# Kernel optimization log

Measured on AMD Instinct MI355X. Metric: run time of the kernel, lower is better.

## Reference

```python
import jax, jax.numpy as jnp
import numpy as np

K_NEIGHBORS = 3  # init kwarg k_neighbors


def setup_inputs() -> dict:
    key = jax.random.key(0)
    k1, k2 = jax.random.split(key)
    q = jax.random.normal(k1, (75, 640, 21, 21), dtype=jnp.float32)
    S = jax.random.normal(k2, (5, 640, 21, 21), dtype=jnp.float32)
    return {"q": q, "S": S, "qAV_num": 1, "SAV_num": 1, "shot_num": 1}


def reference(q, S, qAV_num, SAV_num, shot_num):
    B, C = q.shape[0], q.shape[1]
    # [B, HW, C], L2-normalize each local descriptor over channels
    qd = q.reshape(B, C, -1).transpose(0, 2, 1)
    qd = qd / jnp.linalg.norm(qd, axis=2, keepdims=True)

    N = S.shape[0]
    sd = S.reshape(N, C, -1).transpose(0, 2, 1)  # [N, HW, C]
    sd = sd / jnp.linalg.norm(sd, axis=2, keepdims=True)
    HW = sd.shape[1]
    M = SAV_num * shot_num * HW
    # group support images into classes: [ncls, C, M]
    sup = sd.reshape(-1, M, C).transpose(0, 2, 1)
    ncls = sup.shape[0]

    # cosine similarity: [B, ncls, HW, M]
    ip = jnp.einsum('bqc,ncm->bnqm', qd, sup)
    # split AV groups: [B//qAV, qAV, ncls, HW, M]
    ip = ip.reshape(B // qAV_num, qAV_num, ncls, HW, M)
    # top-k along the query-descriptor (HW) axis (torch dim=-2)
    topk = jax.lax.top_k(jnp.swapaxes(ip, -1, -2), K_NEIGHBORS)[0]  # [..., M, k]
    img2class = topk.sum(axis=(-1, -2))  # [B', qAV, ncls]
    # geometric mean over the AV axis (dim=1)
    sim = jnp.exp(jnp.mean(jnp.log(img2class), axis=1))  # [B', ncls]
    return sim
```

## Files before the change

### kernel.cpp

```cpp
#include <hip/hip_runtime.h>
#include <hip/hip_bf16.h>


#define B_IMGS 75
#define N_CLS  5
#define C_DIM  640
#define HW     441
#define HWP    448
#define NKT    20
#define NRB    28
#define CHUNK  512

typedef __attribute__((ext_vector_type(8))) short  short8;
typedef __attribute__((ext_vector_type(4))) float  float4v;

__device__ __forceinline__ void ins3(float& t0, float& t1, float& t2, float v) {
    float m  = fminf(t0, v);
    t0 = fmaxf(t0, v);
    float m2 = fminf(t1, m);
    t1 = fmaxf(t1, m);
    t2 = fmaxf(t2, m2);
}

__global__ __launch_bounds__(256)
void prep_kernel(const float* __restrict__ q, const float* __restrict__ S,
                 __hip_bfloat16* __restrict__ qn2, __hip_bfloat16* __restrict__ sn2,
                 float* __restrict__ out) {
    __shared__ float part[4][64];
    __shared__ float inv[64];

    int bid = blockIdx.x;
    if (bid == 0) {
        for (int i = threadIdx.x; i < B_IMGS * N_CLS; i += 256) out[i] = 0.f;
    }

    int img = bid / 7;
    int h0  = bid % 7;
    const float* src; __hip_bfloat16* dst;
    if (img < B_IMGS) {
        src = q + (size_t)img * C_DIM * HW;
        dst = qn2 + (size_t)img * NRB * NKT * CHUNK;
    } else {
        src = S + (size_t)(img - B_IMGS) * C_DIM * HW;
        dst = sn2 + (size_t)(img - B_IMGS) * NRB * NKT * CHUNK;
    }
    int t  = threadIdx.x;
    int hl = t & 63;
    int p  = t >> 6;
    int hw = h0 * 64 + hl;
    int hwc = (hw < HW) ? hw : (HW - 1);

    float ss = 0.f;
    for (int c0 = p * 160; c0 < (p + 1) * 160; c0 += 16) {
        float v[16];
#pragma unroll
        for (int j = 0; j < 16; ++j) v[j] = src[(size_t)(c0 + j) * HW + hwc];
#pragma unroll
        for (int j = 0; j < 16; ++j) ss += v[j] * v[j];
    }
    part[p][hl] = ss;
    __syncthreads();
    if (t < 64) {
        float tot = part[0][t] + part[1][t] + part[2][t] + part[3][t];
        inv[t] = (h0 * 64 + t < HW) ? rsqrtf(tot) : 0.f;
    }
    __syncthreads();

    int tl  = hl;
    int row = tl & 15;
    int oct = tl >> 4;
    int rb  = h0 * 4 + p;
    int hw2 = h0 * 64 + p * 16 + row;
    int hw2c = (hw2 < HW) ? hw2 : (HW - 1);
    float iv = inv[p * 16 + row];
    const float* s2 = src + hw2c;
#pragma unroll 2
    for (int kt = 0; kt < NKT; ++kt) {
        float v[8];
#pragma unroll
        for (int j = 0; j < 8; ++j)
            v[j] = s2[(size_t)(kt * 32 + oct * 8 + j) * HW];
        short8 o;
#pragma unroll
        for (int j = 0; j < 8; ++j) {
            __hip_bfloat16 h = __float2bfloat16(v[j] * iv);
            o[j] = *(short*)&h;
        }
        *(short8*)(dst + ((size_t)rb * NKT + kt) * CHUNK + tl * 8) = o;
    }
}

#define LOADSET(aS, bS, kt)                                                     \
    {                                                                           \
        _Pragma("unroll")                                                       \
        for (int r = 0; r < 7; ++r)                                             \
            aS[r] = *(const short8*)(pA + ((size_t)(r * 4 + w) * NKT + (kt)) * CHUNK); \
        _Pragma("unroll")                                                       \
        for (int j = 0; j < 4; ++j)                                             \
            bS[j] = *(const short8*)(pB + ((size_t)j * NKT + (kt)) * CHUNK);    \
    }

#define MFMASET(aS, bS)                                                         \
    {                                                                           \
        _Pragma("unroll")                                                       \
        for (int r = 0; r < 7; ++r)                                             \
            _Pragma("unroll")                                                   \
            for (int j = 0; j < 4; ++j)                                         \
                acc[r][j] = __builtin_amdgcn_mfma_f32_16x16x32_bf16(            \
                    aS[r], bS[j], acc[r][j], 0, 0, 0);                          \
    }

__global__ __launch_bounds__(256, 2)
void gemm_top3_kernel(const __hip_bfloat16* __restrict__ qn2,
                      const __hip_bfloat16* __restrict__ sn2,
                      float* __restrict__ out) {
    __shared__ float mrg[4][64][3];

    int id  = blockIdx.x;
    int xcd = id & 7;
    int j8  = id >> 3;
    int b   = (j8 / 35) * 8 + xcd;
    if (b >= B_IMGS) return;
    int inner = j8 % 35;
    int n  = inner / 7;
    int mt = inner % 7;

    int tid  = threadIdx.x;
    int w    = tid >> 6;
    int lane = tid & 63;
    int c16  = lane & 15;
    int quad = lane >> 4;

    const __hip_bfloat16* pA = qn2 + (size_t)b * NRB * NKT * CHUNK + lane * 8;
    const __hip_bfloat16* pB = sn2 + ((size_t)n * NRB + mt * 4) * NKT * CHUNK + lane * 8;

    float4v acc[7][4];
#pragma unroll
    for (int r = 0; r < 7; ++r)
#pragma unroll
        for (int j = 0; j < 4; ++j)
            acc[r][j] = (float4v){0.f, 0.f, 0.f, 0.f};

    short8 a0[7], b0[4], a1[7], b1[4];
    LOADSET(a0, b0, 0)
    for (int kt = 0; kt < NKT; kt += 2) {
        LOADSET(a1, b1, kt + 1)
        MFMASET(a0, b0)
        if (kt + 2 < NKT) LOADSET(a0, b0, kt + 2)
        MFMASET(a1, b1)
    }

    float T0[4], T1[4], T2[4];
#pragma unroll
    for (int j = 0; j < 4; ++j) { T0[j] = -1e30f; T1[j] = -1e30f; T2[j] = -1e30f; }
#pragma unroll
    for (int r = 0; r < 7; ++r)
#pragma unroll
        for (int j = 0; j < 4; ++j)
#pragma unroll
            for (int g = 0; g < 4; ++g) {
                int row = r * 64 + w * 16 + quad * 4 + g;
                float v = (row < HW) ? acc[r][j][g] : -1e30f;
                ins3(T0[j], T1[j], T2[j], v);
            }

#pragma unroll
    for (int j = 0; j < 4; ++j) {
#pragma unroll
        for (int d = 16; d <= 32; d <<= 1) {
            float o0 = __shfl_xor(T0[j], d, 64);
            float o1 = __shfl_xor(T1[j], d, 64);
            float o2 = __shfl_xor(T2[j], d, 64);
            ins3(T0[j], T1[j], T2[j], o0);
            ins3(T0[j], T1[j], T2[j], o1);
            ins3(T0[j], T1[j], T2[j], o2);
        }
    }

    if (quad == 0) {
#pragma unroll
        for (int j = 0; j < 4; ++j) {
            mrg[w][j * 16 + c16][0] = T0[j];
            mrg[w][j * 16 + c16][1] = T1[j];
            mrg[w][j * 16 + c16][2] = T2[j];
        }
    }
    __syncthreads();
    if (tid < 64) {
        int col = tid;
        float t0 = mrg[0][col][0], t1 = mrg[0][col][1], t2 = mrg[0][col][2];
#pragma unroll
        for (int ww = 1; ww < 4; ++ww) {
            ins3(t0, t1, t2, mrg[ww][col][0]);
            ins3(t0, t1, t2, mrg[ww][col][1]);
            ins3(t0, t1, t2, mrg[ww][col][2]);
        }
        float s = (mt * 64 + col < HW) ? (t0 + t1 + t2) : 0.f;
#pragma unroll
        for (int d = 32; d >= 1; d >>= 1) s += __shfl_xor(s, d, 64);
        if (tid == 0) atomicAdd(&out[b * N_CLS + n], s);
    }
}

extern "C" void kernel_launch(void* const* d_in, const int* in_sizes, int n_in,
                              void* d_out, int out_size, void* d_ws, size_t ws_size,
                              hipStream_t stream) {
    const float* q = (const float*)d_in[0];
    const float* S = (const float*)d_in[1];
    float* out = (float*)d_out;

    char* ws = (char*)d_ws;
    size_t off = 0;
    __hip_bfloat16* qn2 = (__hip_bfloat16*)(ws + off);
    off += (size_t)B_IMGS * NRB * NKT * CHUNK * 2;  off = (off + 255) & ~(size_t)255;
    __hip_bfloat16* sn2 = (__hip_bfloat16*)(ws + off);

    prep_kernel<<<dim3(80 * 7), dim3(256), 0, stream>>>(q, S, qn2, sn2, out);
    gemm_top3_kernel<<<dim3(8 * 350), dim3(256), 0, stream>>>(qn2, sn2, out);
}
```

Baseline: 256.2 us.

## Stage shared B tiles in LDS via direct global-to-LDS loads

Previously all four waves loaded the same support (B) fragments from global memory redundantly. B chunks are now copied into a shared LDS buffer in two phases of ten k-steps using global_load_lds, split across the waves, and each wave reads them from LDS. This cuts redundant global/L2 traffic for B but adds __syncthreads barriers, an unpipelined load-then-compute boundary per phase, and 40KB of LDS that may limit occupancy.

```diff
diff --git a/kernel.cpp b/kernel.cpp
--- a/kernel.cpp
+++ b/kernel.cpp
@@ -20,6 +20,12 @@
     float m2 = fminf(t1, m);
     t1 = fmaxf(t1, m);
     t2 = fmaxf(t2, m2);
+}
+
+__device__ __forceinline__ void glds16(const __hip_bfloat16* g, __hip_bfloat16* l) {
+    __builtin_amdgcn_global_load_lds(
+        (const __attribute__((address_space(1))) unsigned int*)g,
+        (__attribute__((address_space(3))) unsigned int*)l, 16, 0, 0);
 }
 
 __global__ __launch_bounds__(256)
@@ -90,14 +96,18 @@
     }
 }
 
-#define LOADSET(aS, bS, kt)                                                     \
+#define LOADA(aS, kt)                                                           \
     {                                                                           \
         _Pragma("unroll")                                                       \
         for (int r = 0; r < 7; ++r)                                             \
             aS[r] = *(const short8*)(pA + ((size_t)(r * 4 + w) * NKT + (kt)) * CHUNK); \
+    }
+
+#define BREAD(bS, k10)                                                          \
+    {                                                                           \
         _Pragma("unroll")                                                       \
         for (int j = 0; j < 4; ++j)                                             \
-            bS[j] = *(const short8*)(pB + ((size_t)j * NKT + (kt)) * CHUNK);    \
+            bS[j] = *(const short8*)(sbuf + ((k10) * 4 + j) * CHUNK + lane * 8);\
     }
 
 #define MFMASET(aS, bS)                                                         \
@@ -114,6 +124,7 @@
 void gemm_top3_kernel(const __hip_bfloat16* __restrict__ qn2,
                       const __hip_bfloat16* __restrict__ sn2,
                       float* __restrict__ out) {
+    __shared__ __hip_bfloat16 sbuf[40 * CHUNK];
     __shared__ float mrg[4][64][3];
 
     int id  = blockIdx.x;
@@ -131,8 +142,8 @@
     int c16  = lane & 15;
     int quad = lane >> 4;
 
-    const __hip_bfloat16* pA = qn2 + (size_t)b * NRB * NKT * CHUNK + lane * 8;
-    const __hip_bfloat16* pB = sn2 + ((size_t)n * NRB + mt * 4) * NKT * CHUNK + lane * 8;
+    const __hip_bfloat16* pA  = qn2 + (size_t)b * NRB * NKT * CHUNK + lane * 8;
+    const __hip_bfloat16* qBb = sn2 + ((size_t)n * NRB + mt * 4) * NKT * CHUNK;
 
     float4v acc[7][4];
 #pragma unroll
@@ -141,13 +152,31 @@
         for (int j = 0; j < 4; ++j)
             acc[r][j] = (float4v){0.f, 0.f, 0.f, 0.f};
 
-    short8 a0[7], b0[4], a1[7], b1[4];
-    LOADSET(a0, b0, 0)
-    for (int kt = 0; kt < NKT; kt += 2) {
-        LOADSET(a1, b1, kt + 1)
-        MFMASET(a0, b0)
-        if (kt + 2 < NKT) LOADSET(a0, b0, kt + 2)
-        MFMASET(a1, b1)
+    short8 a0[7], a1[7], bb0[4], bb1[4];
+
+    for (int ph = 0; ph < 2; ++ph) {
+        __syncthreads();
+#pragma unroll
+        for (int i = 0; i < 10; ++i) {
+            int cid = w * 10 + i;
+            int jb  = cid & 3;
+            int k10 = cid >> 2;
+            glds16(qBb + ((size_t)jb * NKT + ph * 10 + k10) * CHUNK + lane * 8,
+                   sbuf + cid * CHUNK + lane * 8);
+        }
+        __syncthreads();
+
+        int base = ph * 10;
+        LOADA(a0, base)
+#pragma unroll
+        for (int k2 = 0; k2 < 10; k2 += 2) {
+            BREAD(bb0, k2)
+            LOADA(a1, base + k2 + 1)
+            MFMASET(a0, bb0)
+            BREAD(bb1, k2 + 1)
+            if (k2 + 2 < 10) LOADA(a0, base + k2 + 2)
+            MFMASET(a1, bb1)
+        }
     }
 
     float T0[4], T1[4], T2[4];
```

New measurement: 308.7 us. 1.2x slower.
